# Kernel optimization log

Hardware: AMD Instinct MI355X
Metric: run time of the kernel (lower is better)

The kernel has to match this reference:

```python
import jax, jax.numpy as jnp
import numpy as np

D = 1024
H = 16
HD = D // H
FFN = D * 2
EPS = 1e-5


def _layernorm(x, g, b):
    mu = jnp.mean(x, axis=-1, keepdims=True)
    var = jnp.var(x, axis=-1, keepdims=True)
    return (x - mu) * jax.lax.rsqrt(var + EPS) * g + b


def setup_inputs() -> dict:
    key = jax.random.key(0)
    ks = jax.random.split(key, 12)
    s = 1.0 / np.sqrt(D)
    inp = {
        "x": jax.random.normal(ks[0], (2, 2048, D), dtype=jnp.float32),
        "Wq": jax.random.normal(ks[1], (D, D), dtype=jnp.float32) * s,
        "bq": jnp.zeros((D,), jnp.float32),
        "Wk": jax.random.normal(ks[2], (D, D), dtype=jnp.float32) * s,
        "bk": jnp.zeros((D,), jnp.float32),
        "Wv": jax.random.normal(ks[3], (D, D), dtype=jnp.float32) * s,
        "bv": jnp.zeros((D,), jnp.float32),
        "Wo": jax.random.normal(ks[4], (D, D), dtype=jnp.float32) * s,
        "bo": jnp.zeros((D,), jnp.float32),
        "g1": jnp.ones((D,), jnp.float32),
        "b1": jnp.zeros((D,), jnp.float32),
        "W_ff1": jax.random.normal(ks[5], (D, FFN), dtype=jnp.float32) * s,
        "b_ff1": jnp.zeros((FFN,), jnp.float32),
        "W_ff2": jax.random.normal(ks[6], (FFN, D), dtype=jnp.float32) * (1.0 / np.sqrt(FFN)),
        "b_ff2": jnp.zeros((D,), jnp.float32),
        "g2": jnp.ones((D,), jnp.float32),
        "b2": jnp.zeros((D,), jnp.float32),
    }
    return inp


def reference(x, Wq, bq, Wk, bk, Wv, bv, Wo, bo, g1, b1, W_ff1, b_ff1, W_ff2, b_ff2, g2, b2):
    B, S, _ = x.shape
    # QKV projections -> [B, H, S, HD]
    def split_heads(t):
        return t.reshape(B, S, H, HD).transpose(0, 2, 1, 3)
    Q = split_heads(x @ Wq + bq)
    K = split_heads(x @ Wk + bk)
    V = split_heads(x @ Wv + bv)
    scores = jnp.einsum('bhqd,bhkd->bhqk', Q, K) / np.sqrt(HD).astype(np.float32)
    attn = jax.nn.softmax(scores, axis=-1)  # dropout = identity in eval
    ctx = jnp.einsum('bhqk,bhkd->bhqd', attn, V)
    ctx = ctx.transpose(0, 2, 1, 3).reshape(B, S, D)
    x = _layernorm(x + ctx @ Wo + bo, g1, b1)
    h = jax.nn.gelu(x @ W_ff1 + b_ff1, approximate=False)
    x = _layernorm(x + h @ W_ff2 + b_ff2, g2, b2)
    return x
```

## Files before the change

### kernel.cpp

```cpp
#include <hip/hip_runtime.h>

#define SEQ 2048
#define NTOK 4096
#define DM 1024
#define LDQK 3072

typedef __attribute__((ext_vector_type(4))) float f32x4;
typedef __attribute__((ext_vector_type(8))) short short8;
typedef __attribute__((ext_vector_type(4))) short short4v;

__device__ __forceinline__ short f2bf(float f) {
  union { float f; unsigned u; } x; x.f = f;
  unsigned r = x.u + 0x7fffu + ((x.u >> 16) & 1u);
  return (short)(r >> 16);
}

__device__ __forceinline__ float bf2f(short s) {
  union { unsigned u; float f; } x;
  x.u = ((unsigned)(unsigned short)s) << 16;
  return x.f;
}

__device__ __forceinline__ void async_load16(const void* g, void* l) {
  __builtin_amdgcn_global_load_lds(
      (const __attribute__((address_space(1))) void*)g,
      (__attribute__((address_space(3))) void*)l, 16, 0, 0);
}

__global__ void __launch_bounds__(256) prep_all(
    const float* __restrict__ Wq, const float* __restrict__ Wk,
    const float* __restrict__ Wv, const float* __restrict__ Wo,
    const float* __restrict__ Wf1, const float* __restrict__ Wf2,
    const float* __restrict__ x,
    short* __restrict__ Wqkv, short* __restrict__ Wto,
    short* __restrict__ Wtf1, short* __restrict__ Wtf2,
    short* __restrict__ xb) {
  const int z = blockIdx.z;
  const int tx = threadIdx.x, ty = threadIdx.y;
  if (z == 6) {
    int blk = blockIdx.y * 64 + blockIdx.x;
    int i = blk * 256 + ty * 32 + tx;
    f32x4 v = ((const f32x4*)x)[i];
    short4v o;
#pragma unroll
    for (int j = 0; j < 4; ++j) o[j] = f2bf(v[j]);
    ((short4v*)xb)[i] = o;
    return;
  }
  const float* in;
  short* out;
  int K, N;
  switch (z) {
    case 0: in = Wq;  out = Wqkv;               K = 1024; N = 1024; break;
    case 1: in = Wk;  out = Wqkv + 1024 * 1024; K = 1024; N = 1024; break;
    case 2: in = Wv;  out = Wqkv + 2048 * 1024; K = 1024; N = 1024; break;
    case 3: in = Wo;  out = Wto;                K = 1024; N = 1024; break;
    case 4: in = Wf1; out = Wtf1;               K = 1024; N = 2048; break;
    default: in = Wf2; out = Wtf2;              K = 2048; N = 1024; break;
  }
  if (blockIdx.x * 32 >= N || blockIdx.y * 32 >= K) return;
  __shared__ float t[32][33];
  const int n = blockIdx.x * 32 + tx;
#pragma unroll
  for (int i = 0; i < 4; ++i) {
    int k = blockIdx.y * 32 + ty + i * 8;
    t[ty + i * 8][tx] = in[(size_t)k * N + n];
  }
  __syncthreads();
  const int k2 = blockIdx.y * 32 + tx;
#pragma unroll
  for (int i = 0; i < 4; ++i) {
    int n2 = blockIdx.x * 32 + ty + i * 8;
    out[(size_t)n2 * K + k2] = f2bf(t[tx][ty + i * 8]);
  }
}

template <int EPI, bool TRIPLE>
__global__ void __launch_bounds__(256, 2) gemm_bt(
    const short* __restrict__ A, const short* __restrict__ Bt,
    const float* __restrict__ b0, const float* __restrict__ b1,
    const float* __restrict__ b2, void* __restrict__ Cout,
    short* __restrict__ VtOut, int M, int N, int K) {
  __shared__ __align__(16) short As[128 * 64];
  __shared__ __align__(16) short Bs[128 * 64];
  const int w = threadIdx.x >> 6, lane = threadIdx.x & 63;
  const int hi = lane >> 4, lo = lane & 15;
  const int bm = blockIdx.y, bn = blockIdx.x;
  const int wr = w >> 1, wc = w & 1;
  f32x4 acc[4][4] = {};
  const int nkt = K >> 6;
  for (int kt = 0; kt < nkt; ++kt) {
#pragma unroll
    for (int j = 0; j < 4; ++j) {
      int c = (j * 4 + w) * 64 + lane;
      int r = c >> 3;
      int scc = (c & 7) ^ (r & 7);
      async_load16(A + (size_t)(bm * 128 + r) * K + kt * 64 + scc * 8,
                   &As[(j * 4 + w) * 512]);
      async_load16(Bt + (size_t)(bn * 128 + r) * K + kt * 64 + scc * 8,
                   &Bs[(j * 4 + w) * 512]);
    }
    __syncthreads();
#pragma unroll
    for (int ks = 0; ks < 2; ++ks) {
      short8 af[4], bf[4];
#pragma unroll
      for (int m = 0; m < 4; ++m) {
        int row = wr * 64 + m * 16 + lo;
        int ch = (ks * 4 + hi) ^ (row & 7);
        af[m] = *(const short8*)(&As[row * 64 + ch * 8]);
      }
#pragma unroll
      for (int n = 0; n < 4; ++n) {
        int row = wc * 64 + n * 16 + lo;
        int ch = (ks * 4 + hi) ^ (row & 7);
        bf[n] = *(const short8*)(&Bs[row * 64 + ch * 8]);
      }
#pragma unroll
      for (int m = 0; m < 4; ++m)
#pragma unroll
        for (int n = 0; n < 4; ++n)
          acc[m][n] = __builtin_amdgcn_mfma_f32_16x16x32_bf16(af[m], bf[n], acc[m][n], 0, 0, 0);
    }
    __syncthreads();
  }
  const float* bp = b0;
  if (TRIPLE) { int r = bn >> 3; bp = (r == 0) ? b0 : ((r == 1) ? b1 : b2); }
  const int colb = bn * 128 + wc * 64 + lo;
  if (TRIPLE && bn >= 16) {
#pragma unroll
    for (int m = 0; m < 4; ++m) {
      int row0 = bm * 128 + wr * 64 + m * 16 + hi * 4;
      int bb = row0 >> 11, ss = row0 & 2047;
#pragma unroll
      for (int n = 0; n < 4; ++n) {
        int col = colb + n * 16;
        int vdim = col - 2048;
        int hh = vdim >> 6, dd = vdim & 63;
        float bs = bp[vdim];
        short4v t;
#pragma unroll
        for (int j = 0; j < 4; ++j) t[j] = f2bf(acc[m][n][j] + bs);
        *(short4v*)&VtOut[((size_t)(bb * 16 + hh) * 64 + dd) * SEQ + ss] = t;
      }
    }
    return;
  }
#pragma unroll
  for (int m = 0; m < 4; ++m) {
    int row0 = bm * 128 + wr * 64 + m * 16 + hi * 4;
#pragma unroll
    for (int n = 0; n < 4; ++n) {
      int col = colb + n * 16;
      float bs = bp[TRIPLE ? (col & 1023) : col];
#pragma unroll
      for (int j = 0; j < 4; ++j) {
        float v = acc[m][n][j] + bs;
        if (EPI == 1) v = 0.5f * v * (1.f + erff(v * 0.70710678f));
        ((short*)Cout)[(size_t)(row0 + j) * N + col] = f2bf(v);
      }
    }
  }
}

__global__ void __launch_bounds__(256, 2) gemm_n64(
    const short* __restrict__ A, const short* __restrict__ Bt,
    const float* __restrict__ b0, short* __restrict__ Cout,
    int M, int N, int K) {
  __shared__ __align__(16) short As[128 * 64];
  __shared__ __align__(16) short Bs[64 * 64];
  const int w = threadIdx.x >> 6, lane = threadIdx.x & 63;
  const int hi = lane >> 4, lo = lane & 15;
  const int bm = blockIdx.y, bn = blockIdx.x;
  const int wr = w >> 1, wc = w & 1;
  f32x4 acc[4][2] = {};
  const int nkt = K >> 6;
  for (int kt = 0; kt < nkt; ++kt) {
#pragma unroll
    for (int j = 0; j < 4; ++j) {
      int c = (j * 4 + w) * 64 + lane;
      int r = c >> 3;
      int scc = (c & 7) ^ (r & 7);
      async_load16(A + (size_t)(bm * 128 + r) * K + kt * 64 + scc * 8,
                   &As[(j * 4 + w) * 512]);
    }
#pragma unroll
    for (int j = 0; j < 2; ++j) {
      int c = j * 256 + w * 64 + lane;
      int r = c >> 3;
      int scc = (c & 7) ^ (r & 7);
      async_load16(Bt + (size_t)(bn * 64 + r) * K + kt * 64 + scc * 8,
                   &Bs[(j * 256 + w * 64) * 8]);
    }
    __syncthreads();
#pragma unroll
    for (int ks = 0; ks < 2; ++ks) {
      short8 af[4], bf[2];
#pragma unroll
      for (int m = 0; m < 4; ++m) {
        int row = wr * 64 + m * 16 + lo;
        int ch = (ks * 4 + hi) ^ (row & 7);
        af[m] = *(const short8*)(&As[row * 64 + ch * 8]);
      }
#pragma unroll
      for (int n = 0; n < 2; ++n) {
        int row = wc * 32 + n * 16 + lo;
        int ch = (ks * 4 + hi) ^ (row & 7);
        bf[n] = *(const short8*)(&Bs[row * 64 + ch * 8]);
      }
#pragma unroll
      for (int m = 0; m < 4; ++m)
#pragma unroll
        for (int n = 0; n < 2; ++n)
          acc[m][n] = __builtin_amdgcn_mfma_f32_16x16x32_bf16(af[m], bf[n], acc[m][n], 0, 0, 0);
    }
    __syncthreads();
  }
  const int colb = bn * 64 + wc * 32 + lo;
#pragma unroll
  for (int m = 0; m < 4; ++m) {
    int row0 = bm * 128 + wr * 64 + m * 16 + hi * 4;
#pragma unroll
    for (int n = 0; n < 2; ++n) {
      int col = colb + n * 16;
      float bs = b0[col];
#pragma unroll
      for (int j = 0; j < 4; ++j)
        Cout[(size_t)(row0 + j) * N + col] = f2bf(acc[m][n][j] + bs);
    }
  }
}

__global__ void __launch_bounds__(256, 2) attn_kernel(
    const short* __restrict__ Qb, const short* __restrict__ Kb,
    const short* __restrict__ Vt, short* __restrict__ ctx) {
  const int w = threadIdx.x >> 6, lane = threadIdx.x & 63;
  const int hi = lane >> 4, lo = lane & 15;
  const int tid = threadIdx.x;
  const int L = blockIdx.y * 16 + blockIdx.x;
  const int W = (L & 7) * 64 + (L >> 3);
  const int qt = W & 15, bh = W >> 4;
  const int b = bh >> 4, h = bh & 15;
  const int qbase = qt * 128 + w * 32;
  const float C = 0.18033688f;

  __shared__ __align__(16) short Ks[2][128 * 64];
  __shared__ __align__(16) short Vs[2][64 * 128];
  __shared__ __align__(16) short P[4][16 * 128];

  const short* qp = Qb + (size_t)(b * SEQ + qbase + lo) * LDQK + h * 64;
  short8 bq[2][2];
#pragma unroll
  for (int u = 0; u < 2; ++u)
#pragma unroll
    for (int c = 0; c < 2; ++c)
      bq[u][c] = *(const short8*)(qp + (size_t)u * 16 * LDQK + c * 32 + hi * 8);

  const short* kb = Kb + (size_t)(b * SEQ) * LDQK + h * 64;
  const short* vb = Vt + (size_t)bh * 64 * SEQ;

  auto stage = [&](int kt, int buf) {
    const short* kg = kb + (size_t)(kt * 128) * LDQK;
#pragma unroll
    for (int i = 0; i < 4; ++i) {
      int c = i * 256 + tid;
      int r = c >> 3, scc = (c & 7) ^ (r & 7);
      async_load16(kg + (size_t)r * LDQK + scc * 8,
                   &Ks[buf][(i * 256 + w * 64) * 8]);
    }
    const short* vg = vb + kt * 128;
#pragma unroll
    for (int i = 0; i < 4; ++i) {
      int c = i * 256 + tid;
      int r = c >> 4, sc2 = (c & 15) ^ (r & 7);
      async_load16(vg + (size_t)r * SEQ + sc2 * 8,
                   &Vs[buf][(i * 256 + w * 64) * 8]);
    }
  };

  stage(0, 0);
  __syncthreads();

  f32x4 o[2][4] = {};
  float lacc[2] = {0.f, 0.f};
  const int x7 = lo & 7;

  for (int kt = 0; kt < SEQ / 128; ++kt) {
    const int buf = kt & 1;
    if (kt + 1 < SEQ / 128) stage(kt + 1, buf ^ 1);

    f32x4 s[2][8] = {};
#pragma unroll
    for (int g = 0; g < 8; ++g) {
      const short* kr = &Ks[buf][(g * 16 + lo) * 64];
      short8 ka0 = *(const short8*)(kr + ((hi) ^ x7) * 8);
      short8 ka1 = *(const short8*)(kr + ((4 + hi) ^ x7) * 8);
      s[0][g] = __builtin_amdgcn_mfma_f32_16x16x32_bf16(ka0, bq[0][0], s[0][g], 0, 0, 0);
      s[1][g] = __builtin_amdgcn_mfma_f32_16x16x32_bf16(ka0, bq[1][0], s[1][g], 0, 0, 0);
      s[0][g] = __builtin_amdgcn_mfma_f32_16x16x32_bf16(ka1, bq[0][1], s[0][g], 0, 0, 0);
      s[1][g] = __builtin_amdgcn_mfma_f32_16x16x32_bf16(ka1, bq[1][1], s[1][g], 0, 0, 0);
    }
    short8 vv[4][4];
#pragma unroll
    for (int ks = 0; ks < 4; ++ks)
#pragma unroll
      for (int a = 0; a < 4; ++a)
        vv[ks][a] = *(const short8*)(&Vs[buf][(a * 16 + lo) * 128 + (((ks * 4 + hi) ^ x7) * 8)]);
#pragma unroll
    for (int u = 0; u < 2; ++u) {
      float rsg[8];
      short* pbase = &P[w][0];
#pragma unroll
      for (int g = 0; g < 8; ++g) {
        float p0 = exp2f(s[u][g][0] * C);
        float p1 = exp2f(s[u][g][1] * C);
        float p2 = exp2f(s[u][g][2] * C);
        float p3 = exp2f(s[u][g][3] * C);
        rsg[g] = (p0 + p1) + (p2 + p3);
        unsigned w0, w1;
        asm("v_cvt_pk_bf16_f32 %0, %1, %2" : "=v"(w0) : "v"(p0), "v"(p1));
        asm("v_cvt_pk_bf16_f32 %0, %1, %2" : "=v"(w1) : "v"(p2), "v"(p3));
        union { unsigned uu[2]; short4v s4; } cv;
        cv.uu[0] = w0; cv.uu[1] = w1;
        int pc = (2 * g + (hi >> 1)) ^ x7;
        *(short4v*)(pbase + lo * 128 + pc * 8 + (hi & 1) * 4) = cv.s4;
      }
#pragma unroll
      for (int ks = 0; ks < 4; ++ks) {
        int pc = (ks * 4 + hi) ^ x7;
        short8 pa = *(const short8*)(pbase + lo * 128 + pc * 8);
#pragma unroll
        for (int a = 0; a < 4; ++a)
          o[u][a] = __builtin_amdgcn_mfma_f32_16x16x32_bf16(pa, vv[ks][a], o[u][a], 0, 0, 0);
      }
      lacc[u] += ((rsg[0] + rsg[1]) + (rsg[2] + rsg[3])) +
                 ((rsg[4] + rsg[5]) + (rsg[6] + rsg[7]));
    }
    __syncthreads();
  }
#pragma unroll
  for (int u = 0; u < 2; ++u) {
    lacc[u] += __shfl_xor(lacc[u], 16);
    lacc[u] += __shfl_xor(lacc[u], 32);
  }
#pragma unroll
  for (int u = 0; u < 2; ++u)
#pragma unroll
    for (int j = 0; j < 4; ++j) {
      float lj = __shfl(lacc[u], hi * 4 + j);
      float inv = 1.f / lj;
      int row = qbase + u * 16 + hi * 4 + j;
#pragma unroll
      for (int a = 0; a < 4; ++a)
        ctx[(size_t)(b * SEQ + row) * DM + h * 64 + a * 16 + lo] = f2bf(o[u][a][j] * inv);
    }
}

__global__ void __launch_bounds__(256) residual_ln(
    const float* __restrict__ xr, const short* __restrict__ yr,
    const float* __restrict__ g, const float* __restrict__ beta,
    float* __restrict__ outf, short* __restrict__ outb) {
  const int row = blockIdx.x;
  const int t = threadIdx.x;
  const size_t base = (size_t)row * DM;
  f32x4 xv = ((const f32x4*)(xr + base))[t];
  short4v yv4 = ((const short4v*)(yr + base))[t];
  f32x4 v;
#pragma unroll
  for (int j = 0; j < 4; ++j) v[j] = xv[j] + bf2f(yv4[j]);
  float s = v[0] + v[1] + v[2] + v[3];
  float s2 = v[0] * v[0] + v[1] * v[1] + v[2] * v[2] + v[3] * v[3];
#pragma unroll
  for (int off = 1; off < 64; off <<= 1) {
    s += __shfl_xor(s, off);
    s2 += __shfl_xor(s2, off);
  }
  __shared__ float rs[4], rs2[4];
  if ((t & 63) == 0) { rs[t >> 6] = s; rs2[t >> 6] = s2; }
  __syncthreads();
  s = rs[0] + rs[1] + rs[2] + rs[3];
  s2 = rs2[0] + rs2[1] + rs2[2] + rs2[3];
  float mu = s * (1.f / DM);
  float var = s2 * (1.f / DM) - mu * mu;
  float rstd = rsqrtf(var + 1e-5f);
  f32x4 gv = ((const f32x4*)g)[t];
  f32x4 bv = ((const f32x4*)beta)[t];
  f32x4 ov;
#pragma unroll
  for (int j = 0; j < 4; ++j) ov[j] = (v[j] - mu) * rstd * gv[j] + bv[j];
  ((f32x4*)(outf + base))[t] = ov;
  if (outb) {
    short4v sb;
#pragma unroll
    for (int j = 0; j < 4; ++j) sb[j] = f2bf(ov[j]);
    ((short4v*)(outb + base))[t] = sb;
  }
}

extern "C" void kernel_launch(void* const* d_in, const int* in_sizes, int n_in,
                              void* d_out, int out_size, void* d_ws, size_t ws_size,
                              hipStream_t stream) {
  (void)in_sizes; (void)n_in; (void)out_size; (void)ws_size;
  const float* x   = (const float*)d_in[0];
  const float* Wq  = (const float*)d_in[1];
  const float* bq  = (const float*)d_in[2];
  const float* Wk  = (const float*)d_in[3];
  const float* bk  = (const float*)d_in[4];
  const float* Wv  = (const float*)d_in[5];
  const float* bv  = (const float*)d_in[6];
  const float* Wo  = (const float*)d_in[7];
  const float* bo  = (const float*)d_in[8];
  const float* g1  = (const float*)d_in[9];
  const float* b1  = (const float*)d_in[10];
  const float* Wf1 = (const float*)d_in[11];
  const float* bf1 = (const float*)d_in[12];
  const float* Wf2 = (const float*)d_in[13];
  const float* bf2 = (const float*)d_in[14];
  const float* g2  = (const float*)d_in[15];
  const float* b2  = (const float*)d_in[16];

  char* ws = (char*)d_ws;
  const size_t MB = 1u << 20;
  short* Wqkv = (short*)(ws + 0 * MB);
  short* Wto  = (short*)(ws + 6 * MB);
  short* Wtf1 = (short*)(ws + 8 * MB);
  short* Wtf2 = (short*)(ws + 12 * MB);
  short* xb   = (short*)(ws + 16 * MB);
  short* QKV  = (short*)(ws + 24 * MB);
  short* Vt   = (short*)(ws + 48 * MB);
  short* ctxb = (short*)(ws + 56 * MB);
  short* aout = (short*)(ws + 64 * MB);
  float* x1f  = (float*)(ws + 80 * MB);
  short* x1b  = xb;
  short* hb   = QKV;
  short* ffo  = (short*)(ws + 48 * MB);

  prep_all<<<dim3(64, 64, 7), dim3(32, 8), 0, stream>>>(
      Wq, Wk, Wv, Wo, Wf1, Wf2, x, Wqkv, Wto, Wtf1, Wtf2, xb);

  gemm_bt<0, true><<<dim3(24, 32), 256, 0, stream>>>(
      xb, Wqkv, bq, bk, bv, QKV, Vt, NTOK, 3072, 1024);

  attn_kernel<<<dim3(16, 32), 256, 0, stream>>>(QKV, QKV + 1024, Vt, ctxb);

  gemm_n64<<<dim3(16, 32), 256, 0, stream>>>(ctxb, Wto, bo, aout, NTOK, 1024, 1024);
  residual_ln<<<4096, 256, 0, stream>>>(x, aout, g1, b1, x1f, x1b);
  gemm_bt<1, false><<<dim3(16, 32), 256, 0, stream>>>(
      x1b, Wtf1, bf1, bf1, bf1, hb, nullptr, NTOK, 2048, 1024);
  gemm_n64<<<dim3(16, 32), 256, 0, stream>>>(hb, Wtf2, bf2, ffo, NTOK, 1024, 2048);
  residual_ln<<<4096, 256, 0, stream>>>(x1f, ffo, g2, b2, (float*)d_out, nullptr);
}
```

Baseline: 222.2 us.

## Double-buffer LDS tiles in output-projection, FFN2 and FFN1 GEMMs

Adds a two-stage LDS ping-pong to gemm_n64 and to a new DBUF variant of gemm_bt used for the FFN1 GEMM. The next K tile's async global-to-LDS loads are issued before the MFMA work on the current tile, so memory latency can overlap with compute. The barrier at the start of each iteration is removed and the one at the end of the loop is kept. LDS use per block doubles, up to 64 KB for the gemm_bt variant, which could limit occupancy. The QKV GEMM keeps single buffering.

Result: no change. 222.8 us (+0.3%).

```diff
diff --git a/kernel.cpp b/kernel.cpp
--- a/kernel.cpp
+++ b/kernel.cpp
@@ -75,32 +75,48 @@
   }
 }
 
-template <int EPI, bool TRIPLE>
+template <int EPI, bool TRIPLE, bool DBUF>
 __global__ void __launch_bounds__(256, 2) gemm_bt(
     const short* __restrict__ A, const short* __restrict__ Bt,
     const float* __restrict__ b0, const float* __restrict__ b1,
     const float* __restrict__ b2, void* __restrict__ Cout,
     short* __restrict__ VtOut, int M, int N, int K) {
-  __shared__ __align__(16) short As[128 * 64];
-  __shared__ __align__(16) short Bs[128 * 64];
+  __shared__ __align__(16) short As[DBUF ? 2 * 128 * 64 : 128 * 64];
+  __shared__ __align__(16) short Bs[DBUF ? 2 * 128 * 64 : 128 * 64];
   const int w = threadIdx.x >> 6, lane = threadIdx.x & 63;
   const int hi = lane >> 4, lo = lane & 15;
   const int bm = blockIdx.y, bn = blockIdx.x;
   const int wr = w >> 1, wc = w & 1;
   f32x4 acc[4][4] = {};
   const int nkt = K >> 6;
-  for (int kt = 0; kt < nkt; ++kt) {
+
+  auto stage = [&](int kt, int buf) {
 #pragma unroll
     for (int j = 0; j < 4; ++j) {
       int c = (j * 4 + w) * 64 + lane;
       int r = c >> 3;
       int scc = (c & 7) ^ (r & 7);
       async_load16(A + (size_t)(bm * 128 + r) * K + kt * 64 + scc * 8,
-                   &As[(j * 4 + w) * 512]);
+                   &As[buf * (128 * 64) + (j * 4 + w) * 512]);
       async_load16(Bt + (size_t)(bn * 128 + r) * K + kt * 64 + scc * 8,
-                   &Bs[(j * 4 + w) * 512]);
-    }
+                   &Bs[buf * (128 * 64) + (j * 4 + w) * 512]);
+    }
+  };
+
+  if (DBUF) {
+    stage(0, 0);
     __syncthreads();
+  }
+
+  for (int kt = 0; kt < nkt; ++kt) {
+    int buf = 0;
+    if (DBUF) {
+      buf = kt & 1;
+      if (kt + 1 < nkt) stage(kt + 1, buf ^ 1);
+    } else {
+      stage(kt, 0);
+      __syncthreads();
+    }
 #pragma unroll
     for (int ks = 0; ks < 2; ++ks) {
       short8 af[4], bf[4];
@@ -108,13 +124,13 @@
       for (int m = 0; m < 4; ++m) {
         int row = wr * 64 + m * 16 + lo;
         int ch = (ks * 4 + hi) ^ (row & 7);
-        af[m] = *(const short8*)(&As[row * 64 + ch * 8]);
+        af[m] = *(const short8*)(&As[buf * (128 * 64) + row * 64 + ch * 8]);
       }
 #pragma unroll
       for (int n = 0; n < 4; ++n) {
         int row = wc * 64 + n * 16 + lo;
         int ch = (ks * 4 + hi) ^ (row & 7);
-        bf[n] = *(const short8*)(&Bs[row * 64 + ch * 8]);
+        bf[n] = *(const short8*)(&Bs[buf * (128 * 64) + row * 64 + ch * 8]);
       }
 #pragma unroll
       for (int m = 0; m < 4; ++m)
@@ -167,22 +183,23 @@
     const short* __restrict__ A, const short* __restrict__ Bt,
     const float* __restrict__ b0, short* __restrict__ Cout,
     int M, int N, int K) {
-  __shared__ __align__(16) short As[128 * 64];
-  __shared__ __align__(16) short Bs[64 * 64];
+  __shared__ __align__(16) short As[2][128 * 64];
+  __shared__ __align__(16) short Bs[2][64 * 64];
   const int w = threadIdx.x >> 6, lane = threadIdx.x & 63;
   const int hi = lane >> 4, lo = lane & 15;
   const int bm = blockIdx.y, bn = blockIdx.x;
   const int wr = w >> 1, wc = w & 1;
   f32x4 acc[4][2] = {};
   const int nkt = K >> 6;
-  for (int kt = 0; kt < nkt; ++kt) {
+
+  auto stage = [&](int kt, int buf) {
 #pragma unroll
     for (int j = 0; j < 4; ++j) {
       int c = (j * 4 + w) * 64 + lane;
       int r = c >> 3;
       int scc = (c & 7) ^ (r & 7);
       async_load16(A + (size_t)(bm * 128 + r) * K + kt * 64 + scc * 8,
-                   &As[(j * 4 + w) * 512]);
+                   &As[buf][(j * 4 + w) * 512]);
     }
 #pragma unroll
     for (int j = 0; j < 2; ++j) {
@@ -190,9 +207,16 @@
       int r = c >> 3;
       int scc = (c & 7) ^ (r & 7);
       async_load16(Bt + (size_t)(bn * 64 + r) * K + kt * 64 + scc * 8,
-                   &Bs[(j * 256 + w * 64) * 8]);
-    }
-    __syncthreads();
+                   &Bs[buf][(j * 256 + w * 64) * 8]);
+    }
+  };
+
+  stage(0, 0);
+  __syncthreads();
+
+  for (int kt = 0; kt < nkt; ++kt) {
+    const int buf = kt & 1;
+    if (kt + 1 < nkt) stage(kt + 1, buf ^ 1);
 #pragma unroll
     for (int ks = 0; ks < 2; ++ks) {
       short8 af[4], bf[2];
@@ -200,13 +224,13 @@
       for (int m = 0; m < 4; ++m) {
         int row = wr * 64 + m * 16 + lo;
         int ch = (ks * 4 + hi) ^ (row & 7);
-        af[m] = *(const short8*)(&As[row * 64 + ch * 8]);
+        af[m] = *(const short8*)(&As[buf][row * 64 + ch * 8]);
       }
 #pragma unroll
       for (int n = 0; n < 2; ++n) {
         int row = wc * 32 + n * 16 + lo;
         int ch = (ks * 4 + hi) ^ (row & 7);
-        bf[n] = *(const short8*)(&Bs[row * 64 + ch * 8]);
+        bf[n] = *(const short8*)(&Bs[buf][row * 64 + ch * 8]);
       }
 #pragma unroll
       for (int m = 0; m < 4; ++m)
@@ -438,14 +462,14 @@
   prep_all<<<dim3(64, 64, 7), dim3(32, 8), 0, stream>>>(
       Wq, Wk, Wv, Wo, Wf1, Wf2, x, Wqkv, Wto, Wtf1, Wtf2, xb);
 
-  gemm_bt<0, true><<<dim3(24, 32), 256, 0, stream>>>(
+  gemm_bt<0, true, false><<<dim3(24, 32), 256, 0, stream>>>(
       xb, Wqkv, bq, bk, bv, QKV, Vt, NTOK, 3072, 1024);
 
   attn_kernel<<<dim3(16, 32), 256, 0, stream>>>(QKV, QKV + 1024, Vt, ctxb);
 
   gemm_n64<<<dim3(16, 32), 256, 0, stream>>>(ctxb, Wto, bo, aout, NTOK, 1024, 1024);
   residual_ln<<<4096, 256, 0, stream>>>(x, aout, g1, b1, x1f, x1b);
-  gemm_bt<1, false><<<dim3(16, 32), 256, 0, stream>>>(
+  gemm_bt<1, false, true><<<dim3(16, 32), 256, 0, stream>>>(
       x1b, Wtf1, bf1, bf1, bf1, hb, nullptr, NTOK, 2048, 1024);
   gemm_n64<<<dim3(16, 32), 256, 0, stream>>>(hb, Wtf2, bf2, ffo, NTOK, 1024, 2048);
   residual_ln<<<4096, 256, 0, stream>>>(x1f, ffo, g2, b2, (float*)d_out, nullptr);
```
